# Optimization experiments

Hardware: AMD Instinct MI355X
Metric: run time of the kernel (lower is better)

The kernel has to match this reference:

```python
import jax, jax.numpy as jnp
import numpy as np

N_NODES = 50000
N_EDGES = 800000
C = 128
D_IN = 32
T0, T1 = 25000, 25000
OUT = 16


def setup_inputs() -> dict:
    key = jax.random.key(0)
    ks = jax.random.split(key, 16)
    s_in = 1.0 / np.sqrt(D_IN)
    s_c = 1.0 / np.sqrt(C)
    return {
        "feats0": jax.random.normal(ks[0], (T0, D_IN), jnp.float32),
        "feats1": jax.random.normal(ks[1], (T1, D_IN), jnp.float32),
        "enc_w0": jax.random.normal(ks[2], (D_IN, C), jnp.float32) * s_in,
        "enc_b0": jnp.zeros((C,), jnp.float32),
        "enc_w1": jax.random.normal(ks[3], (D_IN, C), jnp.float32) * s_in,
        "enc_b1": jnp.zeros((C,), jnp.float32),
        "w_self0": jax.random.normal(ks[4], (C, C), jnp.float32) * s_c,
        "w_neigh0": jax.random.normal(ks[5], (C, C), jnp.float32) * s_c,
        "b0": jnp.zeros((C,), jnp.float32),
        "w_self1": jax.random.normal(ks[6], (C, C), jnp.float32) * s_c,
        "w_neigh1": jax.random.normal(ks[7], (C, C), jnp.float32) * s_c,
        "b1": jnp.zeros((C,), jnp.float32),
        "head_w": jax.random.normal(ks[8], (C, OUT), jnp.float32) * s_c,
        "head_b": jnp.zeros((OUT,), jnp.float32),
        "node_row_idx": jax.random.randint(ks[9], (N_NODES,), 0, T0 + T1, jnp.int32),
        "edge_index": jax.random.randint(ks[10], (2, N_EDGES), 0, N_NODES, jnp.int32),
    }


def reference(feats0, feats1, enc_w0, enc_b0, enc_w1, enc_b1,
              w_self0, w_neigh0, b0, w_self1, w_neigh1, b1,
              head_w, head_b, node_row_idx, edge_index):
    # Heterogeneous per-table encoding -> [T0+T1, C]
    x0 = feats0 @ enc_w0 + enc_b0
    x1 = feats1 @ enc_w1 + enc_b1
    x_all = jnp.concatenate([x0, x1], axis=0)
    # Irregular gather: each graph node pulls its table row (vectorized form
    # of the Python loop over index_dict/inverse_index_dict in the original)
    x = x_all[node_row_idx]  # [N, C]

    src, dst = edge_index[0], edge_index[1]
    deg = jnp.maximum(
        jax.ops.segment_sum(jnp.ones((N_EDGES,), x.dtype), dst, num_segments=N_NODES),
        1.0)[:, None]

    # GraphSAGE (mean aggr), 2 layers, ReLU between layers
    for ws, wn, bb, act in ((w_self0, w_neigh0, b0, True),
                            (w_self1, w_neigh1, b1, False)):
        agg = jax.ops.segment_sum(x[src], dst, num_segments=N_NODES) / deg
        x = x @ ws + agg @ wn + bb
        if act:
            x = jax.nn.relu(x)

    return x @ head_w + head_b  # [N, OUT]
```

## Files before the change

kernel.cpp:

```cpp
#include <hip/hip_runtime.h>
#include <hip/hip_bf16.h>

#define N_NODES 50000
#define N_EDGES 800000
#define C 128
#define D_IN 32
#define T0 25000
#define OUT_DIM 16
#define NBUCKETS ((N_NODES + 255) / 256)
#define NB1 512
#define CHUNK1 ((N_EDGES + NB1 - 1) / NB1)
#define ENC_BLOCKS 512
#define HIST_BLOCKS 256
#define PREP_ITEMS (2 * 128 * 256 + 2 * 16 * 128)
#define PREP_BLOCKS ((PREP_ITEMS + 255) / 256)


typedef __attribute__((ext_vector_type(8))) short short8;
typedef __attribute__((ext_vector_type(4))) float f32x4;

__device__ __forceinline__ unsigned short f2bf(float f) {
    union { float f; unsigned int i; } u; u.f = f;
    unsigned int x = u.i;
    unsigned int r = x + 0x7fffu + ((x >> 16) & 1u);
    return (unsigned short)(r >> 16);
}
__device__ __forceinline__ float bf2f(unsigned short h) {
    union { unsigned int i; float f; } u; u.i = ((unsigned int)h) << 16;
    return u.f;
}
__device__ __forceinline__ float lo_f(unsigned int w) {
    union { unsigned int i; float f; } u; u.i = w << 16;
    return u.f;
}
__device__ __forceinline__ float hi_f(unsigned int w) {
    union { unsigned int i; float f; } u; u.i = w & 0xffff0000u;
    return u.f;
}
__device__ __forceinline__ void async16(void* lds, const void* g) {
    __builtin_amdgcn_global_load_lds(
        (const __attribute__((address_space(1))) void*)g,
        (__attribute__((address_space(3))) void*)lds, 16, 0, 0);
}
__device__ __forceinline__ void add8(float* a, uint4 v) {
    a[0] += lo_f(v.x); a[1] += hi_f(v.x);
    a[2] += lo_f(v.y); a[3] += hi_f(v.y);
    a[4] += lo_f(v.z); a[5] += hi_f(v.z);
    a[6] += lo_f(v.w); a[7] += hi_f(v.w);
}

__global__ __launch_bounds__(256) void encode_hist_prep_kernel(
    const float* __restrict__ feats0, const float* __restrict__ feats1,
    const float* __restrict__ w0, const float* __restrict__ b0,
    const float* __restrict__ w1, const float* __restrict__ b1,
    const int* __restrict__ row_idx, unsigned short* __restrict__ xh,
    const int* __restrict__ dst, int* __restrict__ bucket_counts,
    const float* __restrict__ ws0, const float* __restrict__ wn0,
    const float* __restrict__ ws1, const float* __restrict__ wn1,
    const float* __restrict__ hw,
    unsigned short* __restrict__ BT0, unsigned short* __restrict__ BT1,
    unsigned short* __restrict__ hwbh, unsigned short* __restrict__ hwbl)
{
    if (blockIdx.x >= ENC_BLOCKS + HIST_BLOCKS) {
        int idx = (blockIdx.x - ENC_BLOCKS - HIST_BLOCKS) * 256 + threadIdx.x;
        const int per_layer = 128 * 256;
        if (idx < 2 * per_layer) {
            int lyr = idx / per_layer;
            int rem = idx - lyr * per_layer;
            int n = rem >> 8;
            int k = rem & 255;
            int seg = k >> 7;
            int ch = k & 127;
            const float* W = (lyr == 0) ? (seg ? wn0 : ws0)
                                        : (seg ? wn1 : ws1);
            (lyr == 0 ? BT0 : BT1)[(size_t)n * 256 + k] =
                f2bf(W[ch * 128 + n]);
            return;
        }
        int jdx = idx - 2 * per_layer;
        if (jdx >= 2 * 16 * 128) return;
        int plane = jdx >> 11;
        int rem = jdx & 2047;
        int n = rem >> 7;
        int k = rem & 127;
        float v = hw[k * OUT_DIM + n];
        unsigned short hi = f2bf(v);
        (plane ? hwbl : hwbh)[n * 136 + k] = plane ? f2bf(v - bf2f(hi)) : hi;
        return;
    }
    if (blockIdx.x >= ENC_BLOCKS) {
        __shared__ int h[NBUCKETS];
        for (int i = threadIdx.x; i < NBUCKETS; i += 256) h[i] = 0;
        __syncthreads();
        int bid = blockIdx.x - ENC_BLOCKS;
        for (int e = bid * 256 + threadIdx.x; e < N_EDGES;
             e += HIST_BLOCKS * 256)
            atomicAdd(&h[dst[e] >> 8], 1);
        __syncthreads();
        for (int i = threadIdx.x; i < NBUCKETS; i += 256)
            if (h[i]) atomicAdd(&bucket_counts[i], h[i]);
        return;
    }

    __shared__ float sw0[D_IN * C];
    __shared__ float sw1[D_IN * C];
    __shared__ float sb0[C];
    __shared__ float sb1[C];
    for (int i = threadIdx.x; i < D_IN * C; i += blockDim.x) {
        sw0[i] = w0[i];
        sw1[i] = w1[i];
    }
    if (threadIdx.x < C) {
        sb0[threadIdx.x] = b0[threadIdx.x];
        sb1[threadIdx.x] = b1[threadIdx.x];
    }
    __syncthreads();

    const int STEP = ENC_BLOCKS * 16;
    int j = threadIdx.x & 15;
    int ln = threadIdx.x >> 4;
    int n = blockIdx.x * 16 + ln;
    int r = (n < N_NODES) ? row_idx[n] : 0;
    for (; n < N_NODES; n += STEP) {
        int nn = n + STEP;
        int rn = (nn < N_NODES) ? row_idx[nn] : 0;
        const float* f = (r < T0) ? (feats0 + (size_t)r * D_IN)
                                  : (feats1 + (size_t)(r - T0) * D_IN);
        const float* W = (r < T0) ? sw0 : sw1;
        const float* B = (r < T0) ? sb0 : sb1;
        float4 f4[8];
#pragma unroll
        for (int i = 0; i < 8; ++i) f4[i] = ((const float4*)f)[i];
        float acc[8];
#pragma unroll
        for (int cc = 0; cc < 8; ++cc) acc[cc] = B[8 * j + cc];
#pragma unroll
        for (int k = 0; k < D_IN; ++k) {
            float fk = ((const float*)f4)[k];
            float4 wa = *(const float4*)&W[k * C + 8 * j];
            float4 wb = *(const float4*)&W[k * C + 8 * j + 4];
            acc[0] += fk * wa.x; acc[1] += fk * wa.y;
            acc[2] += fk * wa.z; acc[3] += fk * wa.w;
            acc[4] += fk * wb.x; acc[5] += fk * wb.y;
            acc[6] += fk * wb.z; acc[7] += fk * wb.w;
        }
        short8 h8;
#pragma unroll
        for (int cc = 0; cc < 8; ++cc) h8[cc] = (short)f2bf(acc[cc]);
        *(short8*)(xh + (size_t)n * 128 + 8 * j) = h8;
        r = rn;
    }
}

__global__ __launch_bounds__(256) void scanb_kernel(
    const int* __restrict__ bucket_counts, int* __restrict__ bucket_base,
    int* __restrict__ bucket_cursor, int* __restrict__ offsets)
{
    __shared__ int ws[4];
    int t = threadIdx.x;
    int c = (t < NBUCKETS) ? bucket_counts[t] : 0;
    int lane = t & 63, wid = t >> 6;
    int v = c;
#pragma unroll
    for (int off = 1; off < 64; off <<= 1) {
        int s = __shfl_up(v, off, 64);
        if (lane >= off) v += s;
    }
    if (lane == 63) ws[wid] = v;
    __syncthreads();
    if (t == 0) {
        int run = 0;
#pragma unroll
        for (int j = 0; j < 4; ++j) { int s = ws[j]; ws[j] = run; run += s; }
    }
    __syncthreads();
    int excl = ws[wid] + (v - c);
    if (t < NBUCKETS) {
        bucket_base[t] = excl;
        bucket_cursor[t] = excl;
    }
    if (t == 0) {
        bucket_base[NBUCKETS] = N_EDGES;
        offsets[N_NODES] = N_EDGES;
    }
}

__global__ __launch_bounds__(256) void bucket1_kernel(
    const int* __restrict__ src, const int* __restrict__ dst,
    int* __restrict__ bucket_cursor, uint2* __restrict__ pairs)
{
    __shared__ int hist[NBUCKETS];
    __shared__ int base[NBUCKETS];
    __shared__ int cur[NBUCKETS];
    int tid = threadIdx.x;
    for (int i = tid; i < NBUCKETS; i += 256) { hist[i] = 0; cur[i] = 0; }
    __syncthreads();
    int ebeg = blockIdx.x * CHUNK1;
    int eend = ebeg + CHUNK1;
    if (eend > N_EDGES) eend = N_EDGES;
    for (int e = ebeg + tid; e < eend; e += 256)
        atomicAdd(&hist[dst[e] >> 8], 1);
    __syncthreads();
    for (int i = tid; i < NBUCKETS; i += 256)
        if (hist[i] > 0) base[i] = atomicAdd(&bucket_cursor[i], hist[i]);
    __syncthreads();
    for (int e = ebeg + tid; e < eend; e += 256) {
        int d = dst[e];
        int b = d >> 8;
        int pos = base[b] + atomicAdd(&cur[b], 1);
        pairs[pos] = make_uint2((unsigned)src[e], (unsigned)d);
    }
}

__global__ __launch_bounds__(256) void bucket2_kernel(
    const uint2* __restrict__ pairs, const int* __restrict__ bucket_base,
    int* __restrict__ offsets, float* __restrict__ deg,
    int* __restrict__ src_sorted)
{
    __shared__ int cnt[256];
    __shared__ int noff[256];
    __shared__ int cur[256];
    __shared__ int ws[4];
    int b = blockIdx.x;
    int n0 = b << 8;
    int tid = threadIdx.x;
    int bb = bucket_base[b];
    int be = bucket_base[b + 1];
    cnt[tid] = 0;
    cur[tid] = 0;
    __syncthreads();
    for (int e = bb + tid; e < be; e += 256)
        atomicAdd(&cnt[pairs[e].y & 255], 1);
    __syncthreads();
    int c = cnt[tid];
    int lane = tid & 63, wid = tid >> 6;
    int v = c;
#pragma unroll
    for (int off = 1; off < 64; off <<= 1) {
        int s = __shfl_up(v, off, 64);
        if (lane >= off) v += s;
    }
    if (lane == 63) ws[wid] = v;
    __syncthreads();
    if (tid == 0) {
        int run = 0;
#pragma unroll
        for (int j = 0; j < 4; ++j) { int s = ws[j]; ws[j] = run; run += s; }
    }
    __syncthreads();
    int o = bb + ws[wid] + (v - c);
    noff[tid] = o;
    int n = n0 + tid;
    if (n < N_NODES) {
        offsets[n] = o;
        deg[n] = (float)(c > 0 ? c : 1);
    }
    __syncthreads();
    for (int e = bb + tid; e < be; e += 256) {
        uint2 p = pairs[e];
        int local = p.y & 255;
        int pos = noff[local] + atomicAdd(&cur[local], 1);
        src_sorted[pos] = (int)p.x;
    }
}

__global__ __launch_bounds__(256) void aggregate_kernel(
    const unsigned short* __restrict__ xh, const int* __restrict__ offsets,
    const int* __restrict__ src_sorted, const float* __restrict__ deg,
    unsigned short* __restrict__ ah)
{
    int wave = (blockIdx.x * blockDim.x + threadIdx.x) >> 6;
    int lane = threadIdx.x & 63;
    if (wave >= N_NODES) return;
    int h = lane >> 4;
    int u = lane & 15;
    int beg = offsets[wave];
    int end = offsets[wave + 1];
    float acc[8];
#pragma unroll
    for (int j = 0; j < 8; ++j) acc[j] = 0.f;

    for (int e = beg; e < end; e += 32) {
        int idx[8], s[8];
#pragma unroll
        for (int t = 0; t < 8; ++t) {
            idx[t] = e + 4 * t + h;
            int cc = idx[t] < end ? idx[t] : beg;
            s[t] = src_sorted[cc];
        }
        uint4 v[8];
#pragma unroll
        for (int t = 0; t < 8; ++t)
            v[t] = *(const uint4*)(xh + (size_t)s[t] * 128 + u * 8);
#pragma unroll
        for (int t = 0; t < 8; ++t)
            if (idx[t] < end) add8(acc, v[t]);
    }

#pragma unroll
    for (int j = 0; j < 8; ++j) {
        acc[j] += __shfl_xor(acc[j], 16);
        acc[j] += __shfl_xor(acc[j], 32);
    }
    if (lane < 16) {
        float inv = 1.0f / deg[wave];
        short8 hv;
#pragma unroll
        for (int j = 0; j < 8; ++j)
            hv[j] = (short)f2bf(acc[j] * inv);
        *(short8*)(ah + (size_t)wave * 128 + u * 8) = hv;
    }
}

#define BM 128
__global__ __launch_bounds__(512) void gemm_mfma(
    unsigned short* __restrict__ xh, const unsigned short* __restrict__ ah,
    const unsigned short* __restrict__ BT, const float* __restrict__ bias,
    int mode,
    const unsigned short* __restrict__ hwbh,
    const unsigned short* __restrict__ hwbl,
    const float* __restrict__ hb, float* __restrict__ out)
{
    __shared__ uint4 smem4[4096];
    char* As = (char*)smem4;
    char* Bs = (char*)smem4 + 32768;
    __shared__ float bias_s[C];
    __shared__ unsigned short hwh_s[16 * 136];
    __shared__ unsigned short hwl_s[16 * 136];
    __shared__ float hb_s[OUT_DIM];

    int tid = threadIdx.x;
    int w = tid >> 6, l = tid & 63;
    int row0 = blockIdx.x * BM;
    if (tid < C) bias_s[tid] = bias[tid];
    if (mode == 2) {
        for (int i = tid; i < 16 * 136; i += 512) {
            hwh_s[i] = hwbh[i];
            hwl_s[i] = hwbl[i];
        }
        if (tid < OUT_DIM) hb_s[tid] = hb[tid];
    }

    f32x4 acc[2][4];
#pragma unroll
    for (int mt = 0; mt < 2; ++mt)
#pragma unroll
        for (int nt = 0; nt < 4; ++nt)
            acc[mt][nt] = (f32x4)(0.f);

    int wm = w & 3;
    int wn = w >> 2;
    int quad = l >> 4;
    int mrow = l & 15;

    for (int c = 0; c < 2; ++c) {
        const char* abase = (const char*)(c == 0 ? xh : ah);
#pragma unroll
        for (int i = 0; i < 4; ++i) {
            int off = i * 8192 + tid * 16;
            int rl = off >> 8;
            int row = row0 + rl;
            if (row > N_NODES - 1) row = N_NODES - 1;
            int u = ((off >> 4) & 15) ^ (rl & 15);
            async16(As + off, abase + (size_t)row * 256 + u * 16);
        }
#pragma unroll
        for (int i = 0; i < 4; ++i) {
            int off = i * 8192 + tid * 16;
            int n = off >> 8;
            int u = ((off >> 4) & 15) ^ (n & 15);
            async16(Bs + off, (const char*)BT + (size_t)n * 512 + c * 256 + u * 16);
        }
        __syncthreads();
#pragma unroll
        for (int ks = 0; ks < 4; ++ks) {
            int cu = ks * 4 + quad;
            int swz = (cu ^ mrow) * 16;
            short8 a0 = *(const short8*)(As + (wm * 32 + mrow) * 256 + swz);
            short8 a1 = *(const short8*)(As + (wm * 32 + 16 + mrow) * 256 + swz);
            short8 b[4];
#pragma unroll
            for (int nt = 0; nt < 4; ++nt)
                b[nt] = *(const short8*)(Bs + (wn * 64 + nt * 16 + mrow) * 256 + swz);
#pragma unroll
            for (int nt = 0; nt < 4; ++nt) {
                acc[0][nt] = __builtin_amdgcn_mfma_f32_16x16x32_bf16(a0, b[nt], acc[0][nt], 0, 0, 0);
                acc[1][nt] = __builtin_amdgcn_mfma_f32_16x16x32_bf16(a1, b[nt], acc[1][nt], 0, 0, 0);
            }
        }
        __syncthreads();
    }

    char* th = (char*)smem4;
    int relu = (mode == 1);
#pragma unroll
    for (int mt = 0; mt < 2; ++mt)
#pragma unroll
        for (int nt = 0; nt < 4; ++nt) {
            int col = wn * 64 + nt * 16 + mrow;
#pragma unroll
            for (int r = 0; r < 4; ++r) {
                int rl = wm * 32 + mt * 16 + quad * 4 + r;
                float v = acc[mt][nt][r] + bias_s[col];
                if (relu) v = fmaxf(v, 0.f);
                int su = (col >> 3) ^ (rl & 15);
                *(unsigned short*)(th + rl * 256 + su * 16 + (col & 7) * 2) =
                    f2bf(v);
            }
        }
    __syncthreads();

    if (mode == 1) {
#pragma unroll
        for (int i = 0; i < 4; ++i) {
            int off = i * 8192 + tid * 16;
            int rl = off >> 8;
            int su = (((off >> 4) & 15) ^ (rl & 15)) * 16;
            int row = row0 + rl;
            if (row < N_NODES)
                *(uint4*)((char*)xh + (size_t)row * 256 + (off & 255)) =
                    *(const uint4*)(th + rl * 256 + su);
        }
    } else {
        f32x4 hacc = (f32x4)(0.f);
        const unsigned short* Bp[2] = {hwh_s, hwl_s};
#pragma unroll
        for (int ps = 0; ps < 2; ++ps) {
#pragma unroll
            for (int ks = 0; ks < 4; ++ks) {
                int su = ((ks * 4 + quad) ^ mrow) * 16;
                short8 a = *(const short8*)(th + (w * 16 + mrow) * 256 + su);
                short8 b = *(const short8*)((const char*)Bp[ps] +
                                            mrow * 272 + ks * 64 + quad * 16);
                hacc = __builtin_amdgcn_mfma_f32_16x16x32_bf16(a, b, hacc, 0, 0, 0);
            }
        }
        float bb = hb_s[mrow];
#pragma unroll
        for (int r = 0; r < 4; ++r) {
            int grow = row0 + w * 16 + quad * 4 + r;
            if (grow < N_NODES)
                out[(size_t)grow * OUT_DIM + mrow] = hacc[r] + bb;
        }
    }
}

extern "C" void kernel_launch(void* const* d_in, const int* in_sizes, int n_in,
                              void* d_out, int out_size, void* d_ws, size_t ws_size,
                              hipStream_t stream)
{
    const float* feats0 = (const float*)d_in[0];
    const float* feats1 = (const float*)d_in[1];
    const float* enc_w0 = (const float*)d_in[2];
    const float* enc_b0 = (const float*)d_in[3];
    const float* enc_w1 = (const float*)d_in[4];
    const float* enc_b1 = (const float*)d_in[5];
    const float* w_self0 = (const float*)d_in[6];
    const float* w_neigh0 = (const float*)d_in[7];
    const float* b0 = (const float*)d_in[8];
    const float* w_self1 = (const float*)d_in[9];
    const float* w_neigh1 = (const float*)d_in[10];
    const float* b1 = (const float*)d_in[11];
    const float* head_w = (const float*)d_in[12];
    const float* head_b = (const float*)d_in[13];
    const int* node_row_idx = (const int*)d_in[14];
    const int* edge_index = (const int*)d_in[15];
    const int* e_src = edge_index;
    const int* e_dst = edge_index + N_EDGES;

    char* p = (char*)d_ws;
    unsigned short* xh = (unsigned short*)p;  p += (size_t)N_NODES * C * 2;
    unsigned short* ah = (unsigned short*)p;  p += (size_t)N_NODES * C * 2;
    unsigned short* BT0 = (unsigned short*)p; p += (size_t)128 * 256 * 2;
    unsigned short* BT1 = (unsigned short*)p; p += (size_t)128 * 256 * 2;
    unsigned short* hwbh = (unsigned short*)p; p += (size_t)16 * 136 * 2;
    unsigned short* hwbl = (unsigned short*)p; p += (size_t)16 * 136 * 2;
    float* deg = (float*)p;        p += (size_t)N_NODES * 4;
    int* offsets = (int*)p;        p += (size_t)(N_NODES + 8) * 4;
    int* bucket_counts = (int*)p;  p += (size_t)(NBUCKETS + 8) * 4;
    int* bucket_base = (int*)p;    p += (size_t)(NBUCKETS + 8) * 4;
    int* bucket_cursor = (int*)p;  p += (size_t)(NBUCKETS + 8) * 4;
    int* src_sorted = (int*)p;     p += (size_t)N_EDGES * 4;
    uint2* pairs = (uint2*)ah;

    hipMemsetAsync(bucket_counts, 0, (size_t)(NBUCKETS + 8) * 4, stream);

    encode_hist_prep_kernel<<<ENC_BLOCKS + HIST_BLOCKS + PREP_BLOCKS, 256, 0,
                              stream>>>(
        feats0, feats1, enc_w0, enc_b0, enc_w1, enc_b1, node_row_idx, xh,
        e_dst, bucket_counts,
        w_self0, w_neigh0, w_self1, w_neigh1, head_w, BT0, BT1, hwbh, hwbl);

    scanb_kernel<<<1, 256, 0, stream>>>(bucket_counts, bucket_base,
                                        bucket_cursor, offsets);
    bucket1_kernel<<<NB1, 256, 0, stream>>>(e_src, e_dst, bucket_cursor, pairs);
    bucket2_kernel<<<NBUCKETS, 256, 0, stream>>>(pairs, bucket_base, offsets,
                                                 deg, src_sorted);

    aggregate_kernel<<<(N_NODES * 64 + 255) / 256, 256, 0, stream>>>(
        xh, offsets, src_sorted, deg, ah);
    gemm_mfma<<<(N_NODES + BM - 1) / BM, 512, 0, stream>>>(
        xh, ah, BT0, b0, 1, hwbh, hwbl, head_b, (float*)d_out);

    aggregate_kernel<<<(N_NODES * 64 + 255) / 256, 256, 0, stream>>>(
        xh, offsets, src_sorted, deg, ah);
    gemm_mfma<<<(N_NODES + BM - 1) / BM, 512, 0, stream>>>(
        xh, ah, BT1, b1, 2, hwbh, hwbl, head_b, (float*)d_out);
}
```

Before: 224.9 us.

## Compact edge sort buffers to 16/32-bit and drop the bucket-count memset

Each histogram block now writes its private bucket counts to a per-block array, and the scan kernel sums them. This removes the memset and the global atomics. Edge pairs are packed into one 32-bit word, and sorted source indices are stored as 16-bit values, which cuts the bytes moved during the sort and the aggregation gathers. The aggregation loop now handles 16 edges per step instead of 32, which fits the average degree better but keeps fewer gathers in flight. The 16-bit packing relies on the node count staying below 65536.

```diff
diff --git a/kernel.cpp b/kernel.cpp
--- a/kernel.cpp
+++ b/kernel.cpp
@@ -11,7 +11,7 @@
 #define NB1 512
 #define CHUNK1 ((N_EDGES + NB1 - 1) / NB1)
 #define ENC_BLOCKS 512
-#define HIST_BLOCKS 256
+#define HIST_BLOCKS 64
 #define PREP_ITEMS (2 * 128 * 256 + 2 * 16 * 128)
 #define PREP_BLOCKS ((PREP_ITEMS + 255) / 256)
 
@@ -54,7 +54,7 @@
     const float* __restrict__ w0, const float* __restrict__ b0,
     const float* __restrict__ w1, const float* __restrict__ b1,
     const int* __restrict__ row_idx, unsigned short* __restrict__ xh,
-    const int* __restrict__ dst, int* __restrict__ bucket_counts,
+    const int* __restrict__ dst, int* __restrict__ hist_out,
     const float* __restrict__ ws0, const float* __restrict__ wn0,
     const float* __restrict__ ws1, const float* __restrict__ wn1,
     const float* __restrict__ hw,
@@ -98,7 +98,7 @@
             atomicAdd(&h[dst[e] >> 8], 1);
         __syncthreads();
         for (int i = threadIdx.x; i < NBUCKETS; i += 256)
-            if (h[i]) atomicAdd(&bucket_counts[i], h[i]);
+            hist_out[bid * NBUCKETS + i] = h[i];
         return;
     }
 
@@ -153,12 +153,17 @@
 }
 
 __global__ __launch_bounds__(256) void scanb_kernel(
-    const int* __restrict__ bucket_counts, int* __restrict__ bucket_base,
+    const int* __restrict__ hist_out, int* __restrict__ bucket_base,
     int* __restrict__ bucket_cursor, int* __restrict__ offsets)
 {
     __shared__ int ws[4];
     int t = threadIdx.x;
-    int c = (t < NBUCKETS) ? bucket_counts[t] : 0;
+    int c = 0;
+    if (t < NBUCKETS) {
+#pragma unroll 4
+        for (int jb = 0; jb < HIST_BLOCKS; ++jb)
+            c += hist_out[jb * NBUCKETS + t];
+    }
     int lane = t & 63, wid = t >> 6;
     int v = c;
 #pragma unroll
@@ -171,7 +176,7 @@
     if (t == 0) {
         int run = 0;
 #pragma unroll
-        for (int j = 0; j < 4; ++j) { int s = ws[j]; ws[j] = run; run += s; }
+        for (int jj = 0; jj < 4; ++jj) { int s = ws[jj]; ws[jj] = run; run += s; }
     }
     __syncthreads();
     int excl = ws[wid] + (v - c);
@@ -187,7 +192,7 @@
 
 __global__ __launch_bounds__(256) void bucket1_kernel(
     const int* __restrict__ src, const int* __restrict__ dst,
-    int* __restrict__ bucket_cursor, uint2* __restrict__ pairs)
+    int* __restrict__ bucket_cursor, unsigned int* __restrict__ pairs)
 {
     __shared__ int hist[NBUCKETS];
     __shared__ int base[NBUCKETS];
@@ -208,14 +213,14 @@
         int d = dst[e];
         int b = d >> 8;
         int pos = base[b] + atomicAdd(&cur[b], 1);
-        pairs[pos] = make_uint2((unsigned)src[e], (unsigned)d);
+        pairs[pos] = ((unsigned)(d & 255) << 16) | (unsigned)src[e];
     }
 }
 
 __global__ __launch_bounds__(256) void bucket2_kernel(
-    const uint2* __restrict__ pairs, const int* __restrict__ bucket_base,
+    const unsigned int* __restrict__ pairs, const int* __restrict__ bucket_base,
     int* __restrict__ offsets, float* __restrict__ deg,
-    int* __restrict__ src_sorted)
+    unsigned short* __restrict__ src_sorted)
 {
     __shared__ int cnt[256];
     __shared__ int noff[256];
@@ -230,7 +235,7 @@
     cur[tid] = 0;
     __syncthreads();
     for (int e = bb + tid; e < be; e += 256)
-        atomicAdd(&cnt[pairs[e].y & 255], 1);
+        atomicAdd(&cnt[pairs[e] >> 16], 1);
     __syncthreads();
     int c = cnt[tid];
     int lane = tid & 63, wid = tid >> 6;
@@ -245,7 +250,7 @@
     if (tid == 0) {
         int run = 0;
 #pragma unroll
-        for (int j = 0; j < 4; ++j) { int s = ws[j]; ws[j] = run; run += s; }
+        for (int jj = 0; jj < 4; ++jj) { int s = ws[jj]; ws[jj] = run; run += s; }
     }
     __syncthreads();
     int o = bb + ws[wid] + (v - c);
@@ -257,17 +262,17 @@
     }
     __syncthreads();
     for (int e = bb + tid; e < be; e += 256) {
-        uint2 p = pairs[e];
-        int local = p.y & 255;
+        unsigned int p = pairs[e];
+        int local = p >> 16;
         int pos = noff[local] + atomicAdd(&cur[local], 1);
-        src_sorted[pos] = (int)p.x;
+        src_sorted[pos] = (unsigned short)(p & 0xffffu);
     }
 }
 
 __global__ __launch_bounds__(256) void aggregate_kernel(
     const unsigned short* __restrict__ xh, const int* __restrict__ offsets,
-    const int* __restrict__ src_sorted, const float* __restrict__ deg,
-    unsigned short* __restrict__ ah)
+    const unsigned short* __restrict__ src_sorted,
+    const float* __restrict__ deg, unsigned short* __restrict__ ah)
 {
     int wave = (blockIdx.x * blockDim.x + threadIdx.x) >> 6;
     int lane = threadIdx.x & 63;
@@ -276,25 +281,25 @@
     int u = lane & 15;
     int beg = offsets[wave];
     int end = offsets[wave + 1];
+    float dgv = deg[wave];
     float acc[8];
 #pragma unroll
     for (int j = 0; j < 8; ++j) acc[j] = 0.f;
 
-    for (int e = beg; e < end; e += 32) {
-        int idx[8], s[8];
-#pragma unroll
-        for (int t = 0; t < 8; ++t) {
-            idx[t] = e + 4 * t + h;
-            int cc = idx[t] < end ? idx[t] : beg;
-            s[t] = src_sorted[cc];
-        }
-        uint4 v[8];
-#pragma unroll
-        for (int t = 0; t < 8; ++t)
+    for (int e = beg; e < end; e += 16) {
+        int s[4];
+#pragma unroll
+        for (int t = 0; t < 4; ++t) {
+            int i2 = e + 4 * t + h;
+            s[t] = src_sorted[i2 < end ? i2 : beg];
+        }
+        uint4 v[4];
+#pragma unroll
+        for (int t = 0; t < 4; ++t)
             v[t] = *(const uint4*)(xh + (size_t)s[t] * 128 + u * 8);
 #pragma unroll
-        for (int t = 0; t < 8; ++t)
-            if (idx[t] < end) add8(acc, v[t]);
+        for (int t = 0; t < 4; ++t)
+            if (e + 4 * t + h < end) add8(acc, v[t]);
     }
 
 #pragma unroll
@@ -303,7 +308,7 @@
         acc[j] += __shfl_xor(acc[j], 32);
     }
     if (lane < 16) {
-        float inv = 1.0f / deg[wave];
+        float inv = 1.0f / dgv;
         short8 hv;
 #pragma unroll
         for (int j = 0; j < 8; ++j)
@@ -477,21 +482,20 @@
     unsigned short* hwbl = (unsigned short*)p; p += (size_t)16 * 136 * 2;
     float* deg = (float*)p;        p += (size_t)N_NODES * 4;
     int* offsets = (int*)p;        p += (size_t)(N_NODES + 8) * 4;
-    int* bucket_counts = (int*)p;  p += (size_t)(NBUCKETS + 8) * 4;
+    int* hist_out = (int*)p;       p += (size_t)(HIST_BLOCKS * NBUCKETS + 8) * 4;
     int* bucket_base = (int*)p;    p += (size_t)(NBUCKETS + 8) * 4;
     int* bucket_cursor = (int*)p;  p += (size_t)(NBUCKETS + 8) * 4;
-    int* src_sorted = (int*)p;     p += (size_t)N_EDGES * 4;
-    uint2* pairs = (uint2*)ah;
-
-    hipMemsetAsync(bucket_counts, 0, (size_t)(NBUCKETS + 8) * 4, stream);
+    unsigned short* src_sorted = (unsigned short*)p;
+    p += (size_t)N_EDGES * 2;
+    unsigned int* pairs = (unsigned int*)ah;
 
     encode_hist_prep_kernel<<<ENC_BLOCKS + HIST_BLOCKS + PREP_BLOCKS, 256, 0,
                               stream>>>(
         feats0, feats1, enc_w0, enc_b0, enc_w1, enc_b1, node_row_idx, xh,
-        e_dst, bucket_counts,
+        e_dst, hist_out,
         w_self0, w_neigh0, w_self1, w_neigh1, head_w, BT0, BT1, hwbh, hwbl);
 
-    scanb_kernel<<<1, 256, 0, stream>>>(bucket_counts, bucket_base,
+    scanb_kernel<<<1, 256, 0, stream>>>(hist_out, bucket_base,
                                         bucket_cursor, offsets);
     bucket1_kernel<<<NB1, 256, 0, stream>>>(e_src, e_dst, bucket_cursor, pairs);
     bucket2_kernel<<<NBUCKETS, 256, 0, stream>>>(pairs, bucket_base, offsets,
```

Measured after the change: 229.0 us. About the same (+1.8%).
